# Kernel tuning notes

Hardware: AMD Instinct MI355X
Metric: run time of the kernel (lower is better)

The kernel has to match this reference:

```python
import jax, jax.numpy as jnp
import numpy as np

jax.config.update('jax_enable_x64', True)

NV = 300000
NT = 1200000

# Lookup tables from GshellHelper buffers
TRIANGLE_TABLE = jnp.asarray(np.array([
    [-1, -1, -1, -1, -1, -1], [1, 0, 2, -1, -1, -1], [4, 0, 3, -1, -1, -1],
    [1, 4, 2, 1, 3, 4], [3, 1, 5, -1, -1, -1], [2, 3, 0, 2, 5, 3],
    [1, 4, 0, 1, 5, 4], [4, 2, 5, -1, -1, -1], [4, 5, 2, -1, -1, -1],
    [4, 1, 0, 4, 5, 1], [3, 2, 0, 3, 5, 2], [1, 3, 5, -1, -1, -1],
    [4, 1, 2, 4, 3, 1], [3, 0, 4, -1, -1, -1], [2, 0, 1, -1, -1, -1],
    [-1, -1, -1, -1, -1, -1]], dtype=np.int64))
NUM_TRIANGLES_TABLE = jnp.asarray(np.array([0, 1, 1, 2, 1, 2, 2, 1, 1, 2, 2, 1, 2, 1, 1, 0], dtype=np.int64))
BASE_TET_EDGES = jnp.asarray(np.array([0, 1, 0, 2, 0, 3, 1, 2, 1, 3, 2, 3], dtype=np.int64))


def setup_inputs() -> dict:
    key = jax.random.key(0)
    k1, k2, k3 = jax.random.split(key, 3)
    pos_nx3 = jax.random.normal(k1, (NV, 3), dtype=jnp.float32)
    sdf_n = jax.random.normal(k2, (NV,), dtype=jnp.float32)
    tet_fx4 = jax.random.randint(k3, (NT, 4), 0, NV, dtype=jnp.int64)
    return {'pos_nx3': pos_nx3, 'sdf_n': sdf_n, 'tet_fx4': tet_fx4}


def _marching_tets(pos_nx3, sdf_n, tet_fx4):
    Nv = pos_nx3.shape[0]
    Nt = tet_fx4.shape[0]
    U = Nt * 6  # max possible unique edges (padded, static)
    sentinel = Nv * Nv  # any real edge code is < Nv*Nv

    occ_n = sdf_n > 0                               # [Nv]
    occ_fx4 = occ_n[tet_fx4]                        # [Nt,4]

    # build the 6 edges of every tet and sort each pair (min, max)
    edges = tet_fx4[:, BASE_TET_EDGES].reshape(-1, 2)   # [Nt*6, 2]
    e0 = jnp.minimum(edges[:, 0], edges[:, 1])
    e1 = jnp.maximum(edges[:, 0], edges[:, 1])
    code = e0 * Nv + e1                                  # [Nt*6] int64 edge key

    # dedup edges (torch.unique(..., return_inverse=True) equivalent, padded)
    uniq, inv = jnp.unique(code, size=U, fill_value=sentinel, return_inverse=True)
    u0 = jnp.clip(uniq // Nv, 0, Nv - 1)
    u1 = jnp.clip(uniq % Nv, 0, Nv - 1)
    real = uniq < sentinel
    crossing = real & (occ_n[u0] != occ_n[u1])           # edges with a sign change

    # compacted index for crossing edges; -1 for non-crossing (as in torch mapping)
    mapping = jnp.where(crossing, jnp.cumsum(crossing.astype(jnp.int64)) - 1, -1)
    idx_map = mapping[inv].reshape(Nt, 6)                # [Nt,6]

    # linear interpolation to the zero crossing:
    # verts = (p0 * (-s1) + p1 * s0) / (s0 - s1)   (matches the torch flip/negate math)
    s0 = sdf_n[u0]
    s1 = sdf_n[u1]
    denom = jnp.where(crossing, s0 - s1, jnp.asarray(1.0, sdf_n.dtype))
    v = (pos_nx3[u0] * (-s1 / denom)[:, None] + pos_nx3[u1] * (s0 / denom)[:, None])

    # scatter interpolated verts to their compacted slots; drop non-crossing
    target = jnp.where(crossing, mapping, U)
    verts = jnp.zeros((U, 3), pos_nx3.dtype).at[target].set(v, mode='drop')

    # per-tet sign pattern -> triangle table lookup
    v_id = jnp.asarray([1, 2, 4, 8], dtype=jnp.int64)
    tetindex = (occ_fx4.astype(jnp.int64) * v_id[None, :]).sum(-1)   # [Nt]
    num_triangles = NUM_TRIANGLES_TABLE[tetindex]                     # [Nt] in {0,1,2}
    tri6 = TRIANGLE_TABLE[tetindex]                                   # [Nt,6]
    face_idx = jnp.take_along_axis(idx_map, jnp.clip(tri6, 0, 5), axis=1).reshape(Nt, 2, 3)
    valid_tri = jnp.arange(2, dtype=jnp.int64)[None, :] < num_triangles[:, None]
    faces = jnp.where(valid_tri[:, :, None], face_idx, -1)            # [Nt,2,3], -1 padded

    return verts, faces, num_triangles, crossing


def reference(pos_nx3, sdf_n, tet_fx4):
    return _marching_tets(pos_nx3, sdf_n, tet_fx4)
```

## Files before the change

### kernel.cpp

```cpp
#include <hip/hip_runtime.h>
#include <stdint.h>

typedef unsigned long long u64;
typedef unsigned int u32;

#define NVERT 300000
#define NTET  1200000
#define NE    (NTET*6)
#define TILE  4096
#define NTILES ((NE + TILE - 1)/TILE)
#define IDXBITS 23
#define IDXMASK ((1u<<IDXBITS)-1)
#define CODESHIFT 24
#define NBUCKS 4688
#define BUCKSHIFT 49

#define PK_GRID 512

#define P1_TPB  1024
#define P1_KPT  32
#define P1_KEYS (P1_TPB*P1_KPT)
#define P1_GRID ((NE + P1_KEYS - 1)/P1_KEYS)

#define BSHIFT 16
#define BSZ    65536
#define NBUCK  110
#define BPB    8
#define STAGECAP 2240

#define VERTS_OFF 0
#define FACES_OFF 21600000
#define NUMT_OFF  28800000
#define CROSS_OFF 30000000
#define CODES_ELEM 14000000

__constant__ int c_ea[6] = {0,0,0,1,1,2};
__constant__ int c_eb[6] = {1,2,3,2,3,3};
__constant__ int c_numtri[16] = {0,1,1,2,1,2,2,1,1,2,2,1,2,1,1,0};
__constant__ int c_tritab[16][6] = {
 {-1,-1,-1,-1,-1,-1},{1,0,2,-1,-1,-1},{4,0,3,-1,-1,-1},{1,4,2,1,3,4},
 {3,1,5,-1,-1,-1},{2,3,0,2,5,3},{1,4,0,1,5,4},{4,2,5,-1,-1,-1},
 {4,5,2,-1,-1,-1},{4,1,0,4,5,1},{3,2,0,3,5,2},{1,3,5,-1,-1,-1},
 {4,1,2,4,3,1},{3,0,4,-1,-1,-1},{2,0,1,-1,-1,-1},{-1,-1,-1,-1,-1,-1}};

__device__ __forceinline__ int sw(int j){ return j ^ ((j >> 4) & 15); }

__global__ __launch_bounds__(256) void k_pack(const int* __restrict__ tet, const float* __restrict__ sdf,
                       u64* __restrict__ dst, float* __restrict__ occF, u32* __restrict__ histBlk){
  __shared__ u32 h[NBUCKS];
  __shared__ u64 lk[256*6];
  int tid = threadIdx.x;
  for (int r=tid; r<NBUCKS; r+=256) h[r]=0;
  __syncthreads();
  for (int t0 = blockIdx.x*256; t0 < NTET; t0 += PK_GRID*256){
    int t = t0 + tid;
    if (t < NTET){
      int4 q = ((const int4*)tet)[t];
      int v[4] = {q.x, q.y, q.z, q.w};
      u32 o[4];
      int occ = 0;
      #pragma unroll
      for (int j=0;j<4;j++){ o[j] = sdf[v[j]] > 0.f ? 1u : 0u; occ |= (int)o[j] << j; }
      occF[t] = (float)occ;
      u64 base = (u64)t*6;
      #pragma unroll
      for (int k=0;k<6;k++){
        int a = v[c_ea[k]], b = v[c_eb[k]];
        u64 cross = (o[c_ea[k]] != o[c_eb[k]]) ? 1ull : 0ull;
        int e0 = min(a,b), e1 = max(a,b);
        u64 code = ((u64)e0 << 19) | (u64)e1;
        u64 key = (code << CODESHIFT) | (cross << IDXBITS) | (base + (u64)k);
        lk[tid*6+k] = key;
        atomicAdd(&h[(u32)(key >> BUCKSHIFT)], 1u);
      }
    }
    __syncthreads();
    int nt = NTET - t0; if (nt > 256) nt = 256;
    size_t ob = (size_t)t0*6;
    for (int j=tid; j<nt*6; j+=256) dst[ob + j] = lk[j];
    __syncthreads();
  }
  u32* row = histBlk + (size_t)blockIdx.x * NBUCKS;
  for (int r=tid; r<NBUCKS; r+=256) row[r] = h[r];
}

__global__ void k_reduce_hist(const u32* __restrict__ histBlk, u32* __restrict__ hist){
  int b = blockIdx.x*256 + threadIdx.x;
  if (b >= NBUCKS) return;
  u32 s = 0;
  for (int r=0;r<PK_GRID;r++) s += histBlk[(size_t)r*NBUCKS + b];
  hist[b] = s;
}

__global__ void k_psd(const float* __restrict__ pos, const float* __restrict__ sdf,
                      float4* __restrict__ psd){
  int v = blockIdx.x*blockDim.x + threadIdx.x;
  if (v < NVERT) psd[v] = make_float4(pos[3*v], pos[3*v+1], pos[3*v+2], sdf[v]);
}

__global__ void k_fillm1(float4* __restrict__ p, int n4){
  int i = blockIdx.x*blockDim.x + threadIdx.x;
  if (i < n4) p[i] = make_float4(-1.f,-1.f,-1.f,-1.f);
}

__global__ __launch_bounds__(1024) void k_scan_buckets(const u32* __restrict__ hist,
     u32* __restrict__ boff, u32* __restrict__ gcur){
  __shared__ u32 s[1024];
  int tid = threadIdx.x;
  u32 carry = 0;
  for (int start=0; start<NBUCKS; start+=1024){
    int idx = start + tid;
    u32 x = (idx < NBUCKS) ? hist[idx] : 0;
    s[tid] = x; __syncthreads();
    for (int off=1; off<1024; off<<=1){
      u32 t = (tid >= off) ? s[tid-off] : 0;
      __syncthreads();
      s[tid] += t;
      __syncthreads();
    }
    u32 excl = carry + s[tid] - x;
    if (idx < NBUCKS){ boff[idx] = excl; gcur[idx] = excl; }
    carry += s[1023];
    __syncthreads();
  }
}

__global__ __launch_bounds__(P1_TPB) void k_bucket_scatter(const u64* __restrict__ src,
     u64* __restrict__ dst, u32* __restrict__ gcur){
  __shared__ u32 h[NBUCKS];
  int tid = threadIdx.x;
  for (int r=tid;r<NBUCKS;r+=P1_TPB) h[r]=0;
  __syncthreads();
  size_t gi = (size_t)blockIdx.x*P1_KEYS + (size_t)tid*P1_KPT;
  u64 kk[P1_KPT];
  if (gi + P1_KPT <= NE){
    const ulonglong2* p2 = (const ulonglong2*)(src + gi);
    #pragma unroll
    for (int k2=0;k2<P1_KPT/2;k2++){ ulonglong2 t = p2[k2]; kk[2*k2]=t.x; kk[2*k2+1]=t.y; }
  } else {
    #pragma unroll
    for (int k=0;k<P1_KPT;k++) kk[k] = (gi+k < NE) ? src[gi+k] : ~0ull;
  }
  #pragma unroll
  for (int k=0;k<P1_KPT;k++){
    if (gi+k < NE) atomicAdd(&h[(u32)(kk[k] >> BUCKSHIFT)], 1u);
  }
  __syncthreads();
  for (int r=tid;r<NBUCKS;r+=P1_TPB){
    u32 c = h[r];
    h[r] = c ? atomicAdd(&gcur[r], c) : 0u;
  }
  __syncthreads();
  #pragma unroll
  for (int k=0;k<P1_KPT;k++){
    if (gi+k < NE){
      u32 b = (u32)(kk[k] >> BUCKSHIFT);
      u32 p = atomicAdd(&h[b], 1u);
      dst[p] = kk[k];
    }
  }
}

template<int NK>
__global__ __launch_bounds__(256) void k_sort_bucket(const u64* __restrict__ src,
     u64* __restrict__ dst, const u32* __restrict__ hist, const u32* __restrict__ boff){
  __shared__ u64 keys[NK*256];
  __shared__ u64 wsum[4][2];
  int b = blockIdx.x, tid = threadIdx.x;
  u32 n = hist[b];
  if (n == 0) return;
  if (NK == 4  && n > 1024) return;
  if (NK == 8  && (n <= 1024 || n > 2048)) return;
  if (NK == 16 && n <= 2048) return;
  u32 base = boff[b];
  #pragma unroll
  for (int k=0;k<NK;k++){
    int j = k*256 + tid;
    keys[sw(j)] = (j < (int)n) ? src[base + j] : ~0ull;
  }
  __syncthreads();
  int mywave = tid >> 6;
  #pragma unroll 1
  for (int q=0;q<9;q++){
    int sh = 24 + 3*q;
    u64 myk[NK];
    u64 vpack = 0;
    u64 c0 = 0, c1 = 0;
    #pragma unroll
    for (int k=0;k<NK;k++){
      myk[k] = keys[sw(tid*NK+k)];
      u32 d = (u32)((myk[k] >> sh) & 7);
      vpack |= (u64)d << (3*k);
      u64 inc = 1ull << (16*(d&3));
      c0 += (d & 4) ? 0 : inc;
      c1 += (d & 4) ? inc : 0;
    }
    u64 v0 = c0, v1 = c1;
    #pragma unroll
    for (int off=1; off<64; off<<=1){
      u64 t0 = __shfl_up(v0, off, 64);
      u64 t1 = __shfl_up(v1, off, 64);
      if ((tid & 63) >= off){ v0 += t0; v1 += t1; }
    }
    if ((tid & 63) == 63){ wsum[mywave][0] = v0; wsum[mywave][1] = v1; }
    __syncthreads();
    u64 pre0=0, pre1=0, tot0=0, tot1=0;
    #pragma unroll
    for (int wv=0; wv<4; wv++){
      u64 x0 = wsum[wv][0], x1 = wsum[wv][1];
      if (wv < mywave){ pre0 += x0; pre1 += x1; }
      tot0 += x0; tot1 += x1;
    }
    u64 run0 = v0 + pre0 - c0;
    u64 run1 = v1 + pre1 - c1;
    u64 Bp0 = 0, Bp1 = 0;
    u32 acc = 0;
    #pragma unroll
    for (int b2=0;b2<8;b2++){
      u32 f = (u32)(((b2 < 4 ? tot0 : tot1) >> (16*(b2&3))) & 0xFFFF);
      if (b2 < 4) Bp0 |= (u64)acc << (16*b2);
      else        Bp1 |= (u64)acc << (16*(b2&3));
      acc += f;
    }
    #pragma unroll
    for (int k=0;k<NK;k++){
      u32 d = (u32)((vpack >> (3*k)) & 7);
      u32 s2 = d & 3;
      bool hi = (d & 4) != 0;
      u64 Bsel = hi ? Bp1 : Bp0;
      u64 rsel = hi ? run1 : run0;
      u32 pos = (u32)((Bsel >> (16*s2)) & 0xFFFF) + (u32)((rsel >> (16*s2)) & 0xFFFF);
      u64 inc = 1ull << (16*s2);
      run0 += hi ? 0 : inc;
      run1 += hi ? inc : 0;
      keys[sw((int)pos)] = myk[k];
    }
    __syncthreads();
  }
  #pragma unroll
  for (int k=0;k<NK;k++){
    int j = k*256 + tid;
    if (j < (int)n) dst[base + j] = keys[sw(j)];
  }
}

__global__ __launch_bounds__(256) void k_tilesum(const u64* __restrict__ A, u64* __restrict__ tileSums){
  __shared__ u64 s[256];
  int tid = threadIdx.x;
  int start = blockIdx.x*TILE + tid*16;
  u64 myk[16];
  if (start < NE){
    const ulonglong2* A2 = (const ulonglong2*)(A + start);
    #pragma unroll
    for (int k2=0;k2<8;k2++){ ulonglong2 t = A2[k2]; myk[2*k2]=t.x; myk[2*k2+1]=t.y; }
  } else {
    #pragma unroll
    for (int k=0;k<16;k++) myk[k]=0;
  }
  u64 prev = (start > 0 && start <= NE) ? A[start-1] : ~0ull;
  u32 th=0, tc=0;
  #pragma unroll
  for (int k=0;k<16;k++){
    int i = start + k;
    if (i < NE){
      u64 v = myk[k];
      if ((v>>CODESHIFT) != (prev>>CODESHIFT)){
        th++;
        if ((v>>IDXBITS) & 1ull) tc++;
      }
      prev = v;
    }
  }
  s[tid] = ((u64)th<<32) | (u64)tc;
  __syncthreads();
  for (int off=128; off>0; off>>=1){
    if (tid<off) s[tid]+=s[tid+off];
    __syncthreads();
  }
  if (tid==0) tileSums[blockIdx.x] = s[0];
}

__global__ void k_scan_tiles(u64* __restrict__ tileSums, u64* __restrict__ tileOff){
  __shared__ u64 s[256];
  int tid = threadIdx.x;
  u64 carry=0;
  for (int start=0; start<NTILES; start+=256){
    int idx=start+tid;
    u64 x = (idx<NTILES)? tileSums[idx] : 0;
    s[tid]=x; __syncthreads();
    for (int off=1;off<256;off<<=1){
      u64 t=(tid>=off)?s[tid-off]:0;
      __syncthreads();
      s[tid]+=t;
      __syncthreads();
    }
    u64 incl=s[tid], tot=s[255];
    if (idx<NTILES) tileOff[idx] = carry + incl - x;
    carry += tot;
    __syncthreads();
  }
  if (tid==0) tileOff[NTILES] = carry;
}

__global__ __launch_bounds__(256) void k_emit_light(const u64* __restrict__ A,
     const u64* __restrict__ tileOff, u64* __restrict__ pairs, u32* __restrict__ cursors,
     u64* __restrict__ codes, float* __restrict__ crossing_out){
  __shared__ u64 wsum[4];
  __shared__ u32 cnt[NBUCK], lcur[NBUCK];
  __shared__ u32 lofs[NBUCK+1];
  __shared__ u32 gbase[NBUCK];
  __shared__ u64 stage[STAGECAP];
  int tid=threadIdx.x, blk=blockIdx.x;
  int lane = tid & 63, wv = tid >> 6;
  int start = blk*TILE + tid*16;
  if (tid < NBUCK){ cnt[tid]=0; lcur[tid]=0; }
  u64 myk[16];
  if (start < NE){
    const ulonglong2* A2 = (const ulonglong2*)(A + start);
    #pragma unroll
    for (int k2=0;k2<8;k2++){ ulonglong2 t = A2[k2]; myk[2*k2]=t.x; myk[2*k2+1]=t.y; }
  } else {
    #pragma unroll
    for (int k=0;k<16;k++) myk[k]=0;
  }
  u64 prev = (start > 0 && start <= NE) ? A[start-1] : ~0ull;
  u32 headm=0, crossm=0;
  #pragma unroll
  for (int k=0;k<16;k++){
    int i = start + k;
    if (i<NE){
      u64 v = myk[k];
      if ((v>>CODESHIFT) != (prev>>CODESHIFT)) headm |= 1u<<k;
      if ((v>>IDXBITS) & 1ull) crossm |= 1u<<k;
      prev = v;
    }
  }
  __syncthreads();
  #pragma unroll
  for (int k=0;k<16;k++){
    if ((start+k) < NE && ((crossm>>k)&1u))
      atomicAdd(&cnt[((u32)myk[k] & IDXMASK)>>BSHIFT], 1u);
  }
  u32 th = __popc(headm), tc = __popc(headm & crossm);
  u64 x = ((u64)th<<32)|(u64)tc;
  u64 v = x;
  #pragma unroll
  for (int off=1; off<64; off<<=1){
    u64 t = __shfl_up(v, off, 64);
    if (lane >= off) v += t;
  }
  if (lane == 63) wsum[wv] = v;
  __syncthreads();
  u64 pre = 0;
  #pragma unroll
  for (int w2=0; w2<4; w2++){ u64 s2 = wsum[w2]; if (w2 < wv) pre += s2; }
  u64 excl = v - x + pre;
  if (tid < 64){
    u32 a0 = (2*tid   < NBUCK) ? cnt[2*tid]   : 0;
    u32 a1 = (2*tid+1 < NBUCK) ? cnt[2*tid+1] : 0;
    u32 sp = a0 + a1;
    u32 sv = sp;
    #pragma unroll
    for (int off=1; off<64; off<<=1){
      u32 t = __shfl_up(sv, off, 64);
      if (lane >= off) sv += t;
    }
    u32 basex = sv - sp;
    if (2*tid   < NBUCK) lofs[2*tid]   = basex;
    if (2*tid+1 < NBUCK) lofs[2*tid+1] = basex + a0;
    if (tid == 63) lofs[NBUCK] = sv;
  }
  if (tid < NBUCK) gbase[tid] = atomicAdd(&cursors[tid], cnt[tid]);
  __syncthreads();
  bool use_stage = (lofs[NBUCK] <= STAGECAP);
  u64 baseOff = tileOff[blk] + excl;
  u32 H = (u32)(baseOff>>32);
  u32 C = (u32)(baseOff & 0xFFFFFFFFull);
  #pragma unroll
  for (int k=0;k<16;k++){
    int i = start+k;
    if (i>=NE) break;
    bool head  = (headm>>k)&1u;
    bool cross = (crossm>>k)&1u;
    if (head){ H++; if(cross) C++; }
    if (cross){
      int m = (int)C-1;
      u32 orig = (u32)myk[k] & IDXMASK;
      u32 b = orig>>BSHIFT;
      u32 r = atomicAdd(&lcur[b], 1u);
      u64 pr = ((u64)orig<<32) | (u64)(u32)m;
      if (use_stage) stage[lofs[b] + r] = pr;
      else           pairs[(size_t)b*BSZ + gbase[b] + r] = pr;
    }
    if (head){
      crossing_out[H-1] = cross ? 1.f : 0.f;
      if (cross) codes[C-1] = myk[k]>>CODESHIFT;
    }
  }
  __syncthreads();
  if (use_stage){
    int ncross = (int)lofs[NBUCK];
    for (int j = tid; j < ncross; j += 256){
      u64 pr = stage[j];
      u32 b = (u32)(pr>>32) >> BSHIFT;
      pairs[(size_t)b*BSZ + gbase[b] + (u32)(j - (int)lofs[b])] = pr;
    }
  }
}

__global__ __launch_bounds__(256) void k_verts(const u64* __restrict__ codes,
     const float4* __restrict__ psd, const u64* __restrict__ totptr, float* __restrict__ verts){
  __shared__ u64 dummy[5120];
  u32 ncross = (u32)(totptr[0] & 0xFFFFFFFFull);
  u32 stride = gridDim.x * blockDim.x;
  for (u32 i = blockIdx.x*blockDim.x + threadIdx.x; i < ncross; i += stride){
    u64 code = codes[i];
    u32 u0 = (u32)(code >> 19), u1 = (u32)(code & 0x7FFFFull);
    float4 a = psd[u0], b = psd[u1];
    float denom = a.w - b.w;
    float w0 = (-b.w)/denom, w1 = a.w/denom;
    verts[3*i+0] = a.x*w0 + b.x*w1;
    verts[3*i+1] = a.y*w0 + b.y*w1;
    verts[3*i+2] = a.z*w0 + b.z*w1;
  }
  if ((int)ncross < -1){ dummy[threadIdx.x] = codes[0]; verts[0] = (float)dummy[255]; }
}

__global__ void k_tailzero(const u64* __restrict__ totptr,
                           float* __restrict__ verts, float* __restrict__ cross){
  u64 tot = totptr[0];
  u32 nuniq  = (u32)(tot>>32);
  u32 ncross = (u32)(tot & 0xFFFFFFFFull);
  u32 vstart = 3u*ncross;
  u32 vlen = 21600000u - vstart;
  u32 clen = 7200000u - nuniq;
  u32 stride = gridDim.x * blockDim.x;
  for (u32 i = blockIdx.x*blockDim.x + threadIdx.x; i < vlen; i += stride)
    verts[vstart + i] = 0.f;
  for (u32 i = blockIdx.x*blockDim.x + threadIdx.x; i < clen; i += stride)
    cross[nuniq + i] = 0.f;
}

__global__ void k_map_scatter(const u64* __restrict__ pairs, const u32* __restrict__ cursors,
                              float* __restrict__ mapF){
  int b = blockIdx.x / BPB, sub = blockIdx.x % BPB;
  u32 n = cursors[b];
  const u64* p = pairs + (size_t)b*BSZ;
  for (u32 i = (u32)(sub*256 + threadIdx.x); i < n; i += BPB*256){
    u64 v = p[i];
    mapF[(u32)(v>>32)] = (float)(int)(u32)v;
  }
}

__global__ void k_faces(const float* __restrict__ occF, float* faceRegion, float* __restrict__ numt){
  int t = blockIdx.x*blockDim.x + threadIdx.x;
  if (t>=NTET) return;
  int occ = (int)occF[t];
  int ntri = c_numtri[occ];
  float em[6];
  #pragma unroll
  for (int j=0;j<6;j++) em[j] = faceRegion[t*6+j];
  float f[6];
  #pragma unroll
  for (int j=0;j<6;j++){
    int tri = c_tritab[occ][j];
    f[j] = ((j/3) < ntri) ? em[tri] : -1.f;
  }
  #pragma unroll
  for (int j=0;j<6;j++) faceRegion[t*6+j] = f[j];
  numt[t] = (float)ntri;
}

extern "C" void kernel_launch(void* const* d_in, const int* in_sizes, int n_in,
                              void* d_out, int out_size, void* d_ws, size_t ws_size,
                              hipStream_t stream) {
  const float* pos = (const float*)d_in[0];
  const float* sdf = (const float*)d_in[1];
  const int*   tet = (const int*)d_in[2];
  float* out = (float*)d_out;

  char* w = (char*)d_ws;
  u64* bufA     = (u64*)w;
  u32* hist     = (u32*)(w + 57600000);
  u32* boff     = (u32*)(w + 57618752);
  u32* gcur     = (u32*)(w + 57637504);
  u64* tileSums = (u64*)(w + 57656256);
  u64* tileOff  = (u64*)(w + 57670320);
  u32* cursors  = (u32*)(w + 57684392);
  float4* psd   = (float4*)(w + 57684992);
  u64* pairs_ws = (u64*)(w + 62484992);
  u32* histBlk  = (u32*)pairs_ws;

  u64* bufB  = (u64*)d_out;
  u64* codes = (u64*)(out + CODES_ELEM);

  k_pack<<<PK_GRID, 256, 0, stream>>>(tet, sdf, bufA, out + NUMT_OFF, histBlk);
  k_psd<<<(NVERT+255)/256, 256, 0, stream>>>(pos, sdf, psd);
  k_fillm1<<<(7200000/4 + 255)/256, 256, 0, stream>>>((float4*)(out + FACES_OFF), 7200000/4);

  k_reduce_hist<<<(NBUCKS+255)/256, 256, 0, stream>>>(histBlk, hist);
  k_scan_buckets<<<1, 1024, 0, stream>>>(hist, boff, gcur);

  k_bucket_scatter<<<P1_GRID, P1_TPB, 0, stream>>>(bufA, bufB, gcur);
  k_sort_bucket<4><<<NBUCKS, 256, 0, stream>>>(bufB, bufA, hist, boff);
  k_sort_bucket<8><<<NBUCKS, 256, 0, stream>>>(bufB, bufA, hist, boff);
  k_sort_bucket<16><<<NBUCKS, 256, 0, stream>>>(bufB, bufA, hist, boff);

  k_tilesum<<<NTILES, 256, 0, stream>>>(bufA, tileSums);
  k_scan_tiles<<<1, 256, 0, stream>>>(tileSums, tileOff);

  hipMemsetAsync(cursors, 0, NBUCK*sizeof(u32), stream);

  k_emit_light<<<NTILES, 256, 0, stream>>>(bufA, tileOff, pairs_ws, cursors,
                                           codes, out + CROSS_OFF);

  k_verts<<<1024, 256, 0, stream>>>(codes, psd, tileOff + NTILES, out + VERTS_OFF);
  k_tailzero<<<2048, 256, 0, stream>>>(tileOff + NTILES, out + VERTS_OFF, out + CROSS_OFF);

  k_map_scatter<<<NBUCK*BPB, 256, 0, stream>>>(pairs_ws, cursors, out + FACES_OFF);
  k_faces<<<(NTET+255)/256, 256, 0, stream>>>(out + NUMT_OFF, out + FACES_OFF, out + NUMT_OFF);
}
```

Measured before the change: 527.7 us.

## Fuse run-head counting into bucket sort and emit per bucket

```diff
diff --git a/kernel.cpp b/kernel.cpp
--- a/kernel.cpp
+++ b/kernel.cpp
@@ -7,8 +7,6 @@
 #define NVERT 300000
 #define NTET  1200000
 #define NE    (NTET*6)
-#define TILE  4096
-#define NTILES ((NE + TILE - 1)/TILE)
 #define IDXBITS 23
 #define IDXMASK ((1u<<IDXBITS)-1)
 #define CODESHIFT 24
@@ -17,10 +15,9 @@
 
 #define PK_GRID 512
 
+#define P1_GRID 64
 #define P1_TPB  1024
-#define P1_KPT  32
-#define P1_KEYS (P1_TPB*P1_KPT)
-#define P1_GRID ((NE + P1_KEYS - 1)/P1_KEYS)
+#define P1_LEN  (NE/P1_GRID)
 
 #define BSHIFT 16
 #define BSZ    65536
@@ -131,19 +128,12 @@
   int tid = threadIdx.x;
   for (int r=tid;r<NBUCKS;r+=P1_TPB) h[r]=0;
   __syncthreads();
-  size_t gi = (size_t)blockIdx.x*P1_KEYS + (size_t)tid*P1_KPT;
-  u64 kk[P1_KPT];
-  if (gi + P1_KPT <= NE){
-    const ulonglong2* p2 = (const ulonglong2*)(src + gi);
-    #pragma unroll
-    for (int k2=0;k2<P1_KPT/2;k2++){ ulonglong2 t = p2[k2]; kk[2*k2]=t.x; kk[2*k2+1]=t.y; }
-  } else {
-    #pragma unroll
-    for (int k=0;k<P1_KPT;k++) kk[k] = (gi+k < NE) ? src[gi+k] : ~0ull;
-  }
-  #pragma unroll
-  for (int k=0;k<P1_KPT;k++){
-    if (gi+k < NE) atomicAdd(&h[(u32)(kk[k] >> BUCKSHIFT)], 1u);
+  int base = blockIdx.x * P1_LEN;
+  int end  = base + P1_LEN;
+  for (int i = base + tid*2; i < end; i += P1_TPB*2){
+    ulonglong2 t = *(const ulonglong2*)(src + i);
+    atomicAdd(&h[(u32)(t.x >> BUCKSHIFT)], 1u);
+    atomicAdd(&h[(u32)(t.y >> BUCKSHIFT)], 1u);
   }
   __syncthreads();
   for (int r=tid;r<NBUCKS;r+=P1_TPB){
@@ -151,27 +141,28 @@
     h[r] = c ? atomicAdd(&gcur[r], c) : 0u;
   }
   __syncthreads();
-  #pragma unroll
-  for (int k=0;k<P1_KPT;k++){
-    if (gi+k < NE){
-      u32 b = (u32)(kk[k] >> BUCKSHIFT);
-      u32 p = atomicAdd(&h[b], 1u);
-      dst[p] = kk[k];
-    }
+  for (int i = base + tid*2; i < end; i += P1_TPB*2){
+    ulonglong2 t = *(const ulonglong2*)(src + i);
+    u32 b0 = (u32)(t.x >> BUCKSHIFT), b1 = (u32)(t.y >> BUCKSHIFT);
+    dst[atomicAdd(&h[b0], 1u)] = t.x;
+    dst[atomicAdd(&h[b1], 1u)] = t.y;
   }
 }
 
 template<int NK>
 __global__ __launch_bounds__(256) void k_sort_bucket(const u64* __restrict__ src,
-     u64* __restrict__ dst, const u32* __restrict__ hist, const u32* __restrict__ boff){
+     u64* __restrict__ dst, const u32* __restrict__ hist, const u32* __restrict__ boff,
+     u64* __restrict__ bucketSums){
   __shared__ u64 keys[NK*256];
   __shared__ u64 wsum[4][2];
+  __shared__ u64 red[256];
   int b = blockIdx.x, tid = threadIdx.x;
   u32 n = hist[b];
-  if (n == 0) return;
+  if (NK == 4 && n == 0){ if (tid==0) bucketSums[b] = 0; return; }
   if (NK == 4  && n > 1024) return;
   if (NK == 8  && (n <= 1024 || n > 2048)) return;
-  if (NK == 16 && n <= 2048) return;
+  if (NK == 12 && (n <= 2048 || n > 3072)) return;
+  if (NK == 16 && n <= 3072) return;
   u32 base = boff[b];
   #pragma unroll
   for (int k=0;k<NK;k++){
@@ -237,56 +228,36 @@
     }
     __syncthreads();
   }
+  u32 th=0, tc=0;
   #pragma unroll
   for (int k=0;k<NK;k++){
     int j = k*256 + tid;
-    if (j < (int)n) dst[base + j] = keys[sw(j)];
-  }
-}
-
-__global__ __launch_bounds__(256) void k_tilesum(const u64* __restrict__ A, u64* __restrict__ tileSums){
-  __shared__ u64 s[256];
-  int tid = threadIdx.x;
-  int start = blockIdx.x*TILE + tid*16;
-  u64 myk[16];
-  if (start < NE){
-    const ulonglong2* A2 = (const ulonglong2*)(A + start);
-    #pragma unroll
-    for (int k2=0;k2<8;k2++){ ulonglong2 t = A2[k2]; myk[2*k2]=t.x; myk[2*k2+1]=t.y; }
-  } else {
-    #pragma unroll
-    for (int k=0;k<16;k++) myk[k]=0;
-  }
-  u64 prev = (start > 0 && start <= NE) ? A[start-1] : ~0ull;
-  u32 th=0, tc=0;
-  #pragma unroll
-  for (int k=0;k<16;k++){
-    int i = start + k;
-    if (i < NE){
-      u64 v = myk[k];
-      if ((v>>CODESHIFT) != (prev>>CODESHIFT)){
+    if (j < (int)n){
+      u64 v = keys[sw(j)];
+      dst[base + j] = v;
+      u64 pv = (j==0) ? ~0ull : keys[sw(j-1)];
+      if ((v>>CODESHIFT) != (pv>>CODESHIFT)){
         th++;
         if ((v>>IDXBITS) & 1ull) tc++;
       }
-      prev = v;
-    }
-  }
-  s[tid] = ((u64)th<<32) | (u64)tc;
+    }
+  }
+  red[tid] = ((u64)th<<32) | (u64)tc;
   __syncthreads();
   for (int off=128; off>0; off>>=1){
-    if (tid<off) s[tid]+=s[tid+off];
-    __syncthreads();
-  }
-  if (tid==0) tileSums[blockIdx.x] = s[0];
-}
-
-__global__ void k_scan_tiles(u64* __restrict__ tileSums, u64* __restrict__ tileOff){
+    if (tid<off) red[tid]+=red[tid+off];
+    __syncthreads();
+  }
+  if (tid==0) bucketSums[b] = red[0];
+}
+
+__global__ void k_scan_bsum(const u64* __restrict__ bucketSums, u64* __restrict__ bucketOff){
   __shared__ u64 s[256];
   int tid = threadIdx.x;
   u64 carry=0;
-  for (int start=0; start<NTILES; start+=256){
+  for (int start=0; start<NBUCKS; start+=256){
     int idx=start+tid;
-    u64 x = (idx<NTILES)? tileSums[idx] : 0;
+    u64 x = (idx<NBUCKS)? bucketSums[idx] : 0;
     s[tid]=x; __syncthreads();
     for (int off=1;off<256;off<<=1){
       u64 t=(tid>=off)?s[tid-off]:0;
@@ -295,40 +266,41 @@
       __syncthreads();
     }
     u64 incl=s[tid], tot=s[255];
-    if (idx<NTILES) tileOff[idx] = carry + incl - x;
+    if (idx<NBUCKS) bucketOff[idx] = carry + incl - x;
     carry += tot;
     __syncthreads();
   }
-  if (tid==0) tileOff[NTILES] = carry;
+  if (tid==0) bucketOff[NBUCKS] = carry;
 }
 
 __global__ __launch_bounds__(256) void k_emit_light(const u64* __restrict__ A,
-     const u64* __restrict__ tileOff, u64* __restrict__ pairs, u32* __restrict__ cursors,
+     const u32* __restrict__ hist, const u32* __restrict__ boff,
+     const u64* __restrict__ bucketOff, u64* __restrict__ pairs, u32* __restrict__ cursors,
      u64* __restrict__ codes, float* __restrict__ crossing_out){
   __shared__ u64 wsum[4];
   __shared__ u32 cnt[NBUCK], lcur[NBUCK];
   __shared__ u32 lofs[NBUCK+1];
   __shared__ u32 gbase[NBUCK];
   __shared__ u64 stage[STAGECAP];
-  int tid=threadIdx.x, blk=blockIdx.x;
+  int blk = blockIdx.x, tid = threadIdx.x;
+  u32 n = hist[blk];
+  if (n == 0) return;
+  u32 abase = boff[blk];
   int lane = tid & 63, wv = tid >> 6;
-  int start = blk*TILE + tid*16;
+  int start = tid*16;
   if (tid < NBUCK){ cnt[tid]=0; lcur[tid]=0; }
   u64 myk[16];
-  if (start < NE){
-    const ulonglong2* A2 = (const ulonglong2*)(A + start);
-    #pragma unroll
-    for (int k2=0;k2<8;k2++){ ulonglong2 t = A2[k2]; myk[2*k2]=t.x; myk[2*k2+1]=t.y; }
-  } else {
-    #pragma unroll
-    for (int k=0;k<16;k++) myk[k]=0;
-  }
-  u64 prev = (start > 0 && start <= NE) ? A[start-1] : ~0ull;
-  u32 headm=0, crossm=0;
   #pragma unroll
   for (int k=0;k<16;k++){
     int i = start + k;
-    if (i<NE){
+    myk[k] = (i < (int)n) ? A[abase + i] : 0ull;
+  }
+  u64 prev = (start == 0) ? ~0ull : ((start <= (int)n && start > 0) ? A[abase + start - 1] : 0ull);
+  u32 headm=0, crossm=0;
+  #pragma unroll
+  for (int k=0;k<16;k++){
+    int i = start + k;
+    if (i < (int)n){
       u64 v = myk[k];
       if ((v>>CODESHIFT) != (prev>>CODESHIFT)) headm |= 1u<<k;
       if ((v>>IDXBITS) & 1ull) crossm |= 1u<<k;
@@ -338,7 +310,7 @@
   __syncthreads();
   #pragma unroll
   for (int k=0;k<16;k++){
-    if ((start+k) < NE && ((crossm>>k)&1u))
+    if ((start+k) < (int)n && ((crossm>>k)&1u))
       atomicAdd(&cnt[((u32)myk[k] & IDXMASK)>>BSHIFT], 1u);
   }
   u32 th = __popc(headm), tc = __popc(headm & crossm);
@@ -373,13 +345,13 @@
   if (tid < NBUCK) gbase[tid] = atomicAdd(&cursors[tid], cnt[tid]);
   __syncthreads();
   bool use_stage = (lofs[NBUCK] <= STAGECAP);
-  u64 baseOff = tileOff[blk] + excl;
+  u64 baseOff = bucketOff[blk] + excl;
   u32 H = (u32)(baseOff>>32);
   u32 C = (u32)(baseOff & 0xFFFFFFFFull);
   #pragma unroll
   for (int k=0;k<16;k++){
     int i = start+k;
-    if (i>=NE) break;
+    if (i >= (int)n) break;
     bool head  = (headm>>k)&1u;
     bool cross = (crossm>>k)&1u;
     if (head){ H++; if(cross) C++; }
@@ -480,16 +452,16 @@
   float* out = (float*)d_out;
 
   char* w = (char*)d_ws;
-  u64* bufA     = (u64*)w;
-  u32* hist     = (u32*)(w + 57600000);
-  u32* boff     = (u32*)(w + 57618752);
-  u32* gcur     = (u32*)(w + 57637504);
-  u64* tileSums = (u64*)(w + 57656256);
-  u64* tileOff  = (u64*)(w + 57670320);
-  u32* cursors  = (u32*)(w + 57684392);
-  float4* psd   = (float4*)(w + 57684992);
-  u64* pairs_ws = (u64*)(w + 62484992);
-  u32* histBlk  = (u32*)pairs_ws;
+  u64* bufA       = (u64*)w;
+  u32* hist       = (u32*)(w + 57600000);
+  u32* boff       = (u32*)(w + 57618752);
+  u32* gcur       = (u32*)(w + 57637504);
+  u64* bucketSums = (u64*)(w + 57656256);
+  u64* bucketOff  = (u64*)(w + 57693760);
+  u32* cursors    = (u32*)(w + 57731272);
+  float4* psd     = (float4*)(w + 57731840);
+  u64* pairs_ws   = (u64*)(w + 62531840);
+  u32* histBlk    = (u32*)pairs_ws;
 
   u64* bufB  = (u64*)d_out;
   u64* codes = (u64*)(out + CODES_ELEM);
@@ -502,20 +474,20 @@
   k_scan_buckets<<<1, 1024, 0, stream>>>(hist, boff, gcur);
 
   k_bucket_scatter<<<P1_GRID, P1_TPB, 0, stream>>>(bufA, bufB, gcur);
-  k_sort_bucket<4><<<NBUCKS, 256, 0, stream>>>(bufB, bufA, hist, boff);
-  k_sort_bucket<8><<<NBUCKS, 256, 0, stream>>>(bufB, bufA, hist, boff);
-  k_sort_bucket<16><<<NBUCKS, 256, 0, stream>>>(bufB, bufA, hist, boff);
-
-  k_tilesum<<<NTILES, 256, 0, stream>>>(bufA, tileSums);
-  k_scan_tiles<<<1, 256, 0, stream>>>(tileSums, tileOff);
+  k_sort_bucket<4><<<NBUCKS, 256, 0, stream>>>(bufB, bufA, hist, boff, bucketSums);
+  k_sort_bucket<8><<<NBUCKS, 256, 0, stream>>>(bufB, bufA, hist, boff, bucketSums);
+  k_sort_bucket<12><<<NBUCKS, 256, 0, stream>>>(bufB, bufA, hist, boff, bucketSums);
+  k_sort_bucket<16><<<NBUCKS, 256, 0, stream>>>(bufB, bufA, hist, boff, bucketSums);
+
+  k_scan_bsum<<<1, 256, 0, stream>>>(bucketSums, bucketOff);
 
   hipMemsetAsync(cursors, 0, NBUCK*sizeof(u32), stream);
 
-  k_emit_light<<<NTILES, 256, 0, stream>>>(bufA, tileOff, pairs_ws, cursors,
+  k_emit_light<<<NBUCKS, 256, 0, stream>>>(bufA, hist, boff, bucketOff, pairs_ws, cursors,
                                            codes, out + CROSS_OFF);
 
-  k_verts<<<1024, 256, 0, stream>>>(codes, psd, tileOff + NTILES, out + VERTS_OFF);
-  k_tailzero<<<2048, 256, 0, stream>>>(tileOff + NTILES, out + VERTS_OFF, out + CROSS_OFF);
+  k_verts<<<1024, 256, 0, stream>>>(codes, psd, bucketOff + NBUCKS, out + VERTS_OFF);
+  k_tailzero<<<2048, 256, 0, stream>>>(bucketOff + NBUCKS, out + VERTS_OFF, out + CROSS_OFF);
 
   k_map_scatter<<<NBUCK*BPB, 256, 0, stream>>>(pairs_ws, cursors, out + FACES_OFF);
   k_faces<<<(NTET+255)/256, 256, 0, stream>>>(out + NUMT_OFF, out + FACES_OFF, out + NUMT_OFF);
```

Result: slower. 637.9 us (+20.9%).
